# Performance work log

Hardware: AMD Instinct MI355X
Metric: run time of the kernel (lower is better)

Reference implementation:

```python
import jax, jax.numpy as jnp
import numpy as np

DIM = 1024; H = 16; KVH = 4; HD = 64          # head_dim = DIM // H
I = 2048                                       # intermediate_size = 2*DIM
N = 16                                         # ssm_state_size
DTR = 64                                       # dt_rank = DIM // 16
K = 4                                          # conv kernel
BASE = 10000.0
EPS = 1.1920929e-07                            # torch F.rms_norm default eps (fp32 finfo eps)

def rms_norm(x):
    return x * jax.lax.rsqrt(jnp.mean(x * x, axis=-1, keepdims=True) + EPS)

def rope_tables(S, dims):
    inv = 1.0 / BASE ** (jnp.arange(0, dims, 2, dtype=jnp.float32) / dims)
    f = jnp.outer(jnp.arange(S, dtype=jnp.float32), inv)   # [S, dims//2]
    return jnp.cos(f), jnp.sin(f)

def apply_rope(x, cos, sin):
    half = x.shape[-1] // 2
    x1, x2 = x[..., :half], x[..., half:]
    return jnp.concatenate([x1 * cos + x2 * sin, -x1 * sin + x2 * cos], axis=-1)

def setup_inputs() -> dict:
    key = jax.random.key(0)
    ks = jax.random.split(key, 12)
    B, S = 2, 2048
    def w(k, shape, s=0.02):
        return jax.random.normal(k, shape, jnp.float32) * s
    return {
        "x": jax.random.normal(ks[0], (B, S, DIM), jnp.float32),
        "W_mamba": w(ks[1], (2 * I, DIM)),
        "W_q": w(ks[2], (DIM, DIM)),
        "W_kv": w(ks[3], (2 * KVH * HD, DIM)),
        "q_gain": jnp.full((H,), 1.0, jnp.float32),
        "conv_w": w(ks[4], (I, K), 0.2),
        "conv_b": jnp.zeros((I,), jnp.float32),
        "W_xproj": w(ks[5], (DTR + 2 * N, I)),
        "W_dt": w(ks[6], (I, DTR)),
        "b_dt": w(ks[7], (I,), 0.5),
        "A_log": jnp.log(jnp.broadcast_to(jnp.arange(1, N + 1, dtype=jnp.float32), (I, N))),
        "D": jnp.ones((I,), jnp.float32),
        "W_mamba_out": w(ks[8], (DIM, I)),
        "W_proj": w(ks[9], (DIM, DIM)),
        "merge_alpha": jnp.zeros((1,), jnp.float32),
    }

def reference(x, W_mamba, W_q, W_kv, q_gain, conv_w, conv_b, W_xproj, W_dt, b_dt,
              A_log, D, W_mamba_out, W_proj, merge_alpha):
    B, S, _ = x.shape
    # --- parallel input projection for the mamba branch ---
    mp = x @ W_mamba.T                         # [B,S,2I]
    x_ssm, gate = mp[..., :I], mp[..., I:]
    # --- attention branch (GQA + full RoPE + per-head q gain) ---
    q = (x @ W_q.T).reshape(B, S, H, HD).transpose(0, 2, 1, 3)
    kv = x @ W_kv.T
    k = kv[..., :KVH * HD].reshape(B, S, KVH, HD).transpose(0, 2, 1, 3)
    v = kv[..., KVH * HD:].reshape(B, S, KVH, HD).transpose(0, 2, 1, 3)
    q = rms_norm(q); k = rms_norm(k)
    cos, sin = rope_tables(S, HD)
    q = apply_rope(q, cos, sin)
    k = apply_rope(k, cos, sin)
    q = q * q_gain[None, :, None, None]
    nrep = H // KVH
    k = jnp.repeat(k, nrep, axis=1)
    v = jnp.repeat(v, nrep, axis=1)
    scores = jnp.einsum('bhqd,bhkd->bhqk', q, k) / jnp.sqrt(jnp.float32(HD))
    mask = jnp.tril(jnp.ones((S, S), bool))
    scores = jnp.where(mask, scores, -jnp.inf)
    y = jnp.einsum('bhqk,bhkd->bhqd', jax.nn.softmax(scores, axis=-1), v)
    attn_out = y.transpose(0, 2, 1, 3).reshape(B, S, DIM)
    # --- mamba/SSM branch: causal depthwise conv1d + silu ---
    xc = x_ssm.transpose(0, 2, 1)              # [B,I,S]
    u = jax.lax.conv_general_dilated(xc, conv_w[:, None, :], (1,), [(K - 1, 0)],
                                     dimension_numbers=('NCH', 'OIH', 'NCH'),
                                     feature_group_count=I) + conv_b[None, :, None]
    u = u * jax.nn.sigmoid(u)                  # silu, [B,I,S]
    u_bsi = u.transpose(0, 2, 1)               # [B,S,I]
    params = u_bsi @ W_xproj.T                 # [B,S,DTR+2N]
    dt_low = params[..., :DTR]
    Bm = params[..., DTR:DTR + N]
    Cm = params[..., DTR + N:]
    delta = jax.nn.softplus(dt_low @ W_dt.T + b_dt)   # [B,S,I] (delta_bias + softplus)
    A = -jnp.exp(A_log)                        # [I,N]
    def step(state, inp):
        d_t, b_t, c_t, u_t = inp               # [B,I],[B,N],[B,N],[B,I]
        dA = jnp.exp(d_t[:, :, None] * A[None])
        state = state * dA + d_t[:, :, None] * b_t[:, None, :] * u_t[:, :, None]
        y_t = jnp.sum(state * c_t[:, None, :], axis=-1)
        return state, y_t
    xs = (delta.transpose(1, 0, 2), Bm.transpose(1, 0, 2),
          Cm.transpose(1, 0, 2), u_bsi.transpose(1, 0, 2))
    state0 = jnp.zeros((B, I, N), x.dtype)
    _, ys = jax.lax.scan(step, state0, xs)     # ys: [S,B,I]
    y_ssm = ys.transpose(1, 0, 2) + u_bsi * D  # + D skip
    y_ssm = y_ssm * (gate * jax.nn.sigmoid(gate))      # gated by silu(z)
    mamba_out = y_ssm @ W_mamba_out.T          # [B,S,DIM]
    # --- gated merge + output projection ---
    alpha = jax.nn.sigmoid(merge_alpha)
    merged = alpha * attn_out + (1.0 - alpha) * mamba_out
    return merged @ W_proj.T
```

## Files before the change

kernel.cpp:

```cpp
#include <hip/hip_runtime.h>
#include <hip/hip_bf16.h>

#define B_   2
#define S_   2048
#define T_   4096
#define DIM_ 1024
#define H_   16
#define KVH_ 4
#define HD_  64
#define I_   2048
#define N_   16
#define DTR_ 64
#define MB   ((size_t)1 << 20)

typedef __hip_bfloat16 bf16;
typedef __attribute__((ext_vector_type(8))) short short8;
typedef __attribute__((ext_vector_type(4))) short short4v;
typedef __attribute__((ext_vector_type(4))) float f32x4;

__device__ __forceinline__ float b2f(bf16 v){ return __bfloat162float(v); }
__device__ __forceinline__ bf16  f2b(float v){ return __float2bfloat16(v); }

__device__ __forceinline__ void async16(const void* g, void* l) {
  __builtin_amdgcn_global_load_lds((__attribute__((address_space(1))) void*)g,
                                   (__attribute__((address_space(3))) void*)l, 16, 0, 0);
}

__global__ __launch_bounds__(256)
void cast_f2b(const float* __restrict__ in, bf16* __restrict__ out, int n4)
{
  const int i = blockIdx.x * 256 + threadIdx.x;
  if (i >= n4) return;
  const float4 v = ((const float4*)in)[i];
  short4v o;
  o.x = (short)__builtin_bit_cast(unsigned short, f2b(v.x));
  o.y = (short)__builtin_bit_cast(unsigned short, f2b(v.y));
  o.z = (short)__builtin_bit_cast(unsigned short, f2b(v.z));
  o.w = (short)__builtin_bit_cast(unsigned short, f2b(v.w));
  *(short4v*)(out + (size_t)i * 4) = o;
}

template<int MODE>
__global__ __launch_bounds__(256)
void gemm_nt(const bf16* __restrict__ A, int lda,
             const bf16* __restrict__ W, int ldw,
             void* __restrict__ C, int ldc,
             const float* __restrict__ bias,
             int M, int N, int K)
{
  __shared__ __align__(16) bf16 As[128*32];
  __shared__ __align__(16) bf16 Bs[128*32];
  const int tid  = threadIdx.x;
  const int lane = tid & 63;
  const int wave = tid >> 6;
  const int l16  = lane & 15;
  const int quad = lane >> 4;
  const int wm   = (wave >> 1) << 6;
  const int wn   = (wave & 1) << 6;
  const int m0   = blockIdx.x << 7;
  const int n0   = blockIdx.y << 7;

  f32x4 acc[4][4];
  const f32x4 zero = {0.f, 0.f, 0.f, 0.f};
  #pragma unroll
  for (int i = 0; i < 4; i++)
    #pragma unroll
    for (int j = 0; j < 4; j++) acc[i][j] = zero;

  for (int k0 = 0; k0 < K; k0 += 32) {
    #pragma unroll
    for (int p = 0; p < 2; p++) {
      const int linear = ((p << 8) + tid) << 4;
      const int row    = linear >> 6;
      const int inrow  = linear & 63;
      async16(A + (size_t)(m0 + row) * lda + k0 + (inrow >> 1), (char*)As + linear);
      int wr = n0 + row; if (wr > N - 1) wr = N - 1;
      async16(W + (size_t)wr * ldw + k0 + (inrow >> 1), (char*)Bs + linear);
    }
    __syncthreads();
    short8 af[4], bfr[4];
    #pragma unroll
    for (int mt = 0; mt < 4; mt++)
      af[mt] = *(const short8*)((const char*)As + ((wm + (mt << 4) + l16) << 6) + (quad << 4));
    #pragma unroll
    for (int nt = 0; nt < 4; nt++)
      bfr[nt] = *(const short8*)((const char*)Bs + ((wn + (nt << 4) + l16) << 6) + (quad << 4));
    #pragma unroll
    for (int mt = 0; mt < 4; mt++)
      #pragma unroll
      for (int nt = 0; nt < 4; nt++)
        acc[mt][nt] = __builtin_amdgcn_mfma_f32_16x16x32_bf16(af[mt], bfr[nt], acc[mt][nt], 0, 0, 0);
    __syncthreads();
  }

  #pragma unroll
  for (int mt = 0; mt < 4; mt++) {
    #pragma unroll
    for (int nt = 0; nt < 4; nt++) {
      const int col = n0 + wn + (nt << 4) + l16;
      if (col >= N) continue;
      #pragma unroll
      for (int r = 0; r < 4; r++) {
        const int row = m0 + wm + (mt << 4) + (quad << 2) + r;
        float v = acc[mt][nt][r];
        if (MODE >= 2) {
          v += bias[col];
          v = (v > 20.f) ? v : log1pf(__expf(v));
        }
        if (MODE == 0 || MODE == 2) ((float*)C)[(size_t)row * ldc + col] = v;
        else                        ((bf16*)C)[(size_t)row * ldc + col] = f2b(v);
      }
    }
  }
}

__global__ __launch_bounds__(256)
void qkv_prep(const bf16* __restrict__ qraw, const bf16* __restrict__ kvraw,
              const float* __restrict__ q_gain,
              bf16* __restrict__ qn, bf16* __restrict__ kn, bf16* __restrict__ vt)
{
  const int wid  = blockIdx.x * 4 + (threadIdx.x >> 6);
  const int lane = threadIdx.x & 63;
  const int t    = wid / 24;
  const int slot = wid % 24;
  const int b = t >> 11, s = t & 2047;

  float val;
  if (slot < 16)       val = b2f(qraw [(size_t)t * 1024 + slot * 64 + lane]);
  else if (slot < 20)  val = b2f(kvraw[(size_t)t * 512  + (slot - 16) * 64 + lane]);
  else                 val = b2f(kvraw[(size_t)t * 512  + 256 + (slot - 20) * 64 + lane]);

  if (slot < 20) {
    float ss = val * val;
    #pragma unroll
    for (int off = 32; off; off >>= 1) ss += __shfl_xor(ss, off);
    val *= rsqrtf(ss * (1.0f / 64.0f) + 1.1920929e-07f);
    const int j = lane & 31;
    const float x1 = __shfl(val, j);
    const float x2 = __shfl(val, j + 32);
    const float inv = powf(10000.0f, -(float)j * (1.0f / 32.0f));
    const float ang = (float)s * inv;
    const float c = cosf(ang), sn = sinf(ang);
    val = (lane < 32) ? (x1 * c + x2 * sn) : (x2 * c - x1 * sn);
  }
  if (slot < 16) {
    val *= q_gain[slot];
    qn[((size_t)(b * 16 + slot) * 2048 + s) * 64 + lane] = f2b(val);
  } else if (slot < 20) {
    kn[((size_t)(b * 4 + (slot - 16)) * 2048 + s) * 64 + lane] = f2b(val);
  } else {
    vt[((size_t)(b * 4 + (slot - 20)) * 64 + lane) * 2048 + s] = f2b(val);
  }
}

__global__ __launch_bounds__(256)
void attn_fwd(const bf16* __restrict__ qn, const bf16* __restrict__ kn,
              const bf16* __restrict__ vt, bf16* __restrict__ attn)
{
  __shared__ __align__(16) bf16 Plds[4][16][32];
  const int b = blockIdx.z, h = blockIdx.y, q0 = blockIdx.x * 64;
  const int wave = threadIdx.x >> 6, lane = threadIdx.x & 63;
  const int l16 = lane & 15, quad = lane >> 4;
  const int kvh = h >> 2;
  const bf16* Q  = qn + (size_t)(b * 16 + h)   * 2048 * 64;
  const bf16* Kp = kn + (size_t)(b * 4 + kvh)  * 2048 * 64;
  const bf16* Vt = vt + (size_t)(b * 4 + kvh)  * 64 * 2048;

  const int qrow_l = q0 + wave * 16 + l16;
  const short8 qf0 = *(const short8*)(Q + (size_t)qrow_l * 64 + quad * 8);
  const short8 qf1 = *(const short8*)(Q + (size_t)qrow_l * 64 + 32 + quad * 8);

  f32x4 acc[4];
  const f32x4 zero = {0.f, 0.f, 0.f, 0.f};
  #pragma unroll
  for (int i = 0; i < 4; i++) acc[i] = zero;
  float m_r[4], l_r[4];
  #pragma unroll
  for (int r = 0; r < 4; r++) { m_r[r] = -1e30f; l_r[r] = 0.f; }

  const int nkt = (q0 + 64) >> 5;
  for (int kt = 0; kt < nkt; kt++) {
    const int kb = kt << 5;
    const short8 kfA0 = *(const short8*)(Kp + (size_t)(kb + l16) * 64 + quad * 8);
    const short8 kfA1 = *(const short8*)(Kp + (size_t)(kb + l16) * 64 + 32 + quad * 8);
    const short8 kfB0 = *(const short8*)(Kp + (size_t)(kb + 16 + l16) * 64 + quad * 8);
    const short8 kfB1 = *(const short8*)(Kp + (size_t)(kb + 16 + l16) * 64 + 32 + quad * 8);
    f32x4 sA = zero, sB = zero;
    sA = __builtin_amdgcn_mfma_f32_16x16x32_bf16(qf0, kfA0, sA, 0, 0, 0);
    sA = __builtin_amdgcn_mfma_f32_16x16x32_bf16(qf1, kfA1, sA, 0, 0, 0);
    sB = __builtin_amdgcn_mfma_f32_16x16x32_bf16(qf0, kfB0, sB, 0, 0, 0);
    sB = __builtin_amdgcn_mfma_f32_16x16x32_bf16(qf1, kfB1, sB, 0, 0, 0);

    const int colA = kb + l16, colB = kb + 16 + l16;
    float pA[4], pB[4], alpha[4];
    #pragma unroll
    for (int r = 0; r < 4; r++) {
      const int row = q0 + wave * 16 + quad * 4 + r;
      float a  = sA[r] * 0.125f;
      float bb = sB[r] * 0.125f;
      if (colA > row) a  = -1e30f;
      if (colB > row) bb = -1e30f;
      float tm = fmaxf(a, bb);
      #pragma unroll
      for (int off = 8; off; off >>= 1) tm = fmaxf(tm, __shfl_xor(tm, off));
      const float nm = fmaxf(m_r[r], tm);
      alpha[r] = __expf(m_r[r] - nm);
      m_r[r] = nm;
      const float pa = __expf(a - nm), pb = __expf(bb - nm);
      pA[r] = pa; pB[r] = pb;
      float ps = pa + pb;
      #pragma unroll
      for (int off = 8; off; off >>= 1) ps += __shfl_xor(ps, off);
      l_r[r] = l_r[r] * alpha[r] + ps;
    }
    #pragma unroll
    for (int nt = 0; nt < 4; nt++)
      #pragma unroll
      for (int r = 0; r < 4; r++) acc[nt][r] *= alpha[r];

    __syncthreads();
    #pragma unroll
    for (int r = 0; r < 4; r++) {
      Plds[wave][quad * 4 + r][l16]      = f2b(pA[r]);
      Plds[wave][quad * 4 + r][16 + l16] = f2b(pB[r]);
    }
    __syncthreads();
    const short8 pf = *(const short8*)(&Plds[wave][l16][quad * 8]);
    #pragma unroll
    for (int nt = 0; nt < 4; nt++) {
      const short8 vf = *(const short8*)(Vt + (size_t)(nt * 16 + l16) * 2048 + kb + quad * 8);
      acc[nt] = __builtin_amdgcn_mfma_f32_16x16x32_bf16(pf, vf, acc[nt], 0, 0, 0);
    }
  }

  #pragma unroll
  for (int nt = 0; nt < 4; nt++)
    #pragma unroll
    for (int r = 0; r < 4; r++) {
      const int row = q0 + wave * 16 + quad * 4 + r;
      attn[((size_t)b * 2048 + row) * 1024 + h * 64 + nt * 16 + l16] = f2b(acc[nt][r] / l_r[r]);
    }
}

__global__ __launch_bounds__(256)
void conv_silu(const bf16* __restrict__ xssm, const float* __restrict__ cw,
               const float* __restrict__ cb, bf16* __restrict__ u)
{
  const int i = blockIdx.x * 256 + threadIdx.x;
  const int t = blockIdx.y;
  const int s = t & 2047;
  float acc = cb[i];
  #pragma unroll
  for (int kk = 0; kk < 4; kk++) {
    const int sp = s - 3 + kk;
    if (sp >= 0) acc += b2f(xssm[(size_t)(t - 3 + kk) * 2048 + i]) * cw[i * 4 + kk];
  }
  const float sig = 1.f / (1.f + __expf(-acc));
  u[(size_t)t * 2048 + i] = f2b(acc * sig);
}

__global__ __launch_bounds__(256)
void ssm_scan(const bf16* __restrict__ delta, const bf16* __restrict__ u,
              const bf16* __restrict__ params, const float* __restrict__ A_log,
              const float* __restrict__ Dv, const bf16* __restrict__ gate,
              bf16* __restrict__ yout)
{
  __shared__ float Pl[16][17], Fl[16][17], Il[16][17];
  const int blk = blockIdx.x;
  const int b = blk >> 11, i = blk & 2047;
  const int n = threadIdx.x & 15, c = threadIdx.x >> 4;
  const float a  = -__expf(A_log[i * 16 + n]);
  const float Di = Dv[i];
  const size_t base = (size_t)b * 2048 + c * 128;

  float P = 1.f, F = 0.f;
  for (int j = 0; j < 128; j++) {
    const size_t rb = base + j;
    const float dt = b2f(delta[rb * 2048 + i]);
    const float ut = b2f(u[rb * 2048 + i]);
    const float Bn = b2f(params[rb * 96 + 64 + n]);
    const float dA = __expf(dt * a);
    P *= dA;
    F = F * dA + dt * ut * Bn;
  }
  Pl[n][c] = P; Fl[n][c] = F;
  __syncthreads();

  if (threadIdx.x < 16) {
    const int nn = threadIdx.x;
    float s = 0.f;
    #pragma unroll
    for (int cc = 0; cc < 16; cc++) {
      Il[nn][cc] = s;
      s = Fl[nn][cc] + Pl[nn][cc] * s;
    }
  }
  __syncthreads();

  float state = Il[n][c];
  for (int j = 0; j < 128; j++) {
    const size_t rb = base + j;
    const float dt = b2f(delta[rb * 2048 + i]);
    const float ut = b2f(u[rb * 2048 + i]);
    const float Bn = b2f(params[rb * 96 + 64 + n]);
    const float Cn = b2f(params[rb * 96 + 80 + n]);
    const float dA = __expf(dt * a);
    state = state * dA + dt * ut * Bn;
    float y = state * Cn;
    y += __shfl_xor(y, 1); y += __shfl_xor(y, 2);
    y += __shfl_xor(y, 4); y += __shfl_xor(y, 8);
    if (n == 0) {
      const float g  = b2f(gate[rb * 2048 + i]);
      const float gs = g / (1.f + __expf(-g));
      yout[rb * 2048 + i] = f2b((y + ut * Di) * gs);
    }
  }
}

__global__ __launch_bounds__(256)
void merge_k(const bf16* __restrict__ attn, const bf16* __restrict__ mamba,
             const float* __restrict__ malpha, bf16* __restrict__ merged)
{
  const size_t idx = (size_t)blockIdx.x * 256 + threadIdx.x;
  const float al = 1.f / (1.f + __expf(-malpha[0]));
  merged[idx] = f2b(al * b2f(attn[idx]) + (1.f - al) * b2f(mamba[idx]));
}

extern "C" void kernel_launch(void* const* d_in, const int* in_sizes, int n_in,
                              void* d_out, int out_size, void* d_ws, size_t ws_size,
                              hipStream_t stream)
{
  const float* x_f     = (const float*)d_in[0];
  const float* Wm_f    = (const float*)d_in[1];
  const float* Wq_f    = (const float*)d_in[2];
  const float* Wkv_f   = (const float*)d_in[3];
  const float* q_gain  = (const float*)d_in[4];
  const float* conv_w  = (const float*)d_in[5];
  const float* conv_b  = (const float*)d_in[6];
  const float* Wxp_f   = (const float*)d_in[7];
  const float* Wdt_f   = (const float*)d_in[8];
  const float* b_dt    = (const float*)d_in[9];
  const float* A_log   = (const float*)d_in[10];
  const float* Dv      = (const float*)d_in[11];
  const float* Wmo_f   = (const float*)d_in[12];
  const float* Wp_f    = (const float*)d_in[13];
  const float* malpha  = (const float*)d_in[14];

  char* wp = (char*)d_ws;
  bf16*  xb    = (bf16*)(wp + 0 * MB);
  bf16*  Wm_b  = (bf16*)(wp + 8 * MB);
  bf16*  Wq_b  = (bf16*)(wp + 16 * MB);
  bf16*  Wkv_b = (bf16*)(wp + 18 * MB);
  bf16*  xssm  = (bf16*)(wp + 19 * MB);
  bf16*  u     = (bf16*)(wp + 35 * MB);
  bf16*  gate  = (bf16*)(wp + 51 * MB);
  bf16*  qraw  = (bf16*)(wp + 67 * MB);
  bf16*  kvraw = (bf16*)(wp + 75 * MB);
  bf16*  dltb  = (bf16*)(wp + 79 * MB);
  bf16*  qn    = (bf16*)(wp + 0 * MB);
  bf16*  kn    = (bf16*)(wp + 8 * MB);
  bf16*  vtb   = (bf16*)(wp + 10 * MB);
  bf16*  Wxp_b = (bf16*)(wp + 12 * MB);
  bf16*  Wdt_b = (bf16*)(wp + 12 * MB + 512 * 1024);
  bf16*  prm   = (bf16*)(wp + 13 * MB);
  bf16*  Wp_b  = (bf16*)(wp + 14 * MB);
  bf16*  attnb = (bf16*)(wp + 67 * MB);
  bf16*  Wmo_b = (bf16*)(wp + 75 * MB);
  bf16*  ybuf  = (bf16*)(wp + 19 * MB);
  bf16*  mam   = (bf16*)(wp + 51 * MB);
  bf16*  mrg   = (bf16*)(wp + 59 * MB);
  (void)ws_size; (void)in_sizes; (void)n_in; (void)out_size;

  auto cast = [&](const float* src, bf16* dst, int n) {
    const int n4 = n >> 2;
    cast_f2b<<<dim3((n4 + 255) / 256), 256, 0, stream>>>(src, dst, n4);
  };
  cast(x_f,   xb,    T_ * 1024);
  cast(Wm_f,  Wm_b,  4096 * 1024);
  cast(Wq_f,  Wq_b,  1024 * 1024);
  cast(Wkv_f, Wkv_b, 512 * 1024);

  gemm_nt<1><<<dim3(32, 16), 256, 0, stream>>>(xb, 1024, Wm_b,               1024, xssm, 2048, nullptr, T_, 2048, 1024);
  gemm_nt<1><<<dim3(32, 16), 256, 0, stream>>>(xb, 1024, Wm_b + 2048 * 1024, 1024, gate, 2048, nullptr, T_, 2048, 1024);
  gemm_nt<1><<<dim3(32, 8),  256, 0, stream>>>(xb, 1024, Wq_b,  1024, qraw,  1024, nullptr, T_, 1024, 1024);
  gemm_nt<1><<<dim3(32, 4),  256, 0, stream>>>(xb, 1024, Wkv_b, 1024, kvraw,  512, nullptr, T_,  512, 1024);

  qkv_prep<<<dim3((T_ * 24) / 4), 256, 0, stream>>>(qraw, kvraw, q_gain, qn, kn, vtb);
  conv_silu<<<dim3(8, 4096), 256, 0, stream>>>(xssm, conv_w, conv_b, u);
  attn_fwd<<<dim3(32, 16, 2), 256, 0, stream>>>(qn, kn, vtb, attnb);

  cast(Wxp_f, Wxp_b, 96 * 2048);
  cast(Wdt_f, Wdt_b, 2048 * 64);
  cast(Wmo_f, Wmo_b, 1024 * 2048);
  cast(Wp_f,  Wp_b,  1024 * 1024);

  gemm_nt<1><<<dim3(32, 1),  256, 0, stream>>>(u, 2048, Wxp_b, 2048, prm, 96, nullptr, T_, 96, 2048);
  gemm_nt<3><<<dim3(32, 16), 256, 0, stream>>>(prm, 96, Wdt_b, 64, dltb, 2048, b_dt, T_, 2048, 64);
  ssm_scan<<<dim3(4096), 256, 0, stream>>>(dltb, u, prm, A_log, Dv, gate, ybuf);
  gemm_nt<1><<<dim3(32, 8),  256, 0, stream>>>(ybuf, 2048, Wmo_b, 2048, mam, 1024, nullptr, T_, 1024, 2048);

  merge_k<<<dim3(16384), 256, 0, stream>>>(attnb, mam, malpha, mrg);
  gemm_nt<0><<<dim3(32, 8),  256, 0, stream>>>(mrg, 1024, Wp_b, 1024, (float*)d_out, 1024, nullptr, T_, 1024, 1024);
}
```

Baseline: 1.046 ms.

## Store SSM scan inputs time-major and vectorize scan loads

```diff
diff --git a/kernel.cpp b/kernel.cpp
--- a/kernel.cpp
+++ b/kernel.cpp
@@ -20,6 +20,12 @@
 
 __device__ __forceinline__ float b2f(bf16 v){ return __bfloat162float(v); }
 __device__ __forceinline__ bf16  f2b(float v){ return __float2bfloat16(v); }
+__device__ __forceinline__ float s2f(short s){
+  return __builtin_bit_cast(float, ((unsigned int)(unsigned short)s) << 16);
+}
+__device__ __forceinline__ short f2s(float v){
+  return (short)__builtin_bit_cast(unsigned short, f2b(v));
+}
 
 __device__ __forceinline__ void async16(const void* g, void* l) {
   __builtin_amdgcn_global_load_lds((__attribute__((address_space(1))) void*)g,
@@ -33,18 +39,16 @@
   if (i >= n4) return;
   const float4 v = ((const float4*)in)[i];
   short4v o;
-  o.x = (short)__builtin_bit_cast(unsigned short, f2b(v.x));
-  o.y = (short)__builtin_bit_cast(unsigned short, f2b(v.y));
-  o.z = (short)__builtin_bit_cast(unsigned short, f2b(v.z));
-  o.w = (short)__builtin_bit_cast(unsigned short, f2b(v.w));
+  o.x = f2s(v.x); o.y = f2s(v.y); o.z = f2s(v.z); o.w = f2s(v.w);
   *(short4v*)(out + (size_t)i * 4) = o;
 }
 
-template<int MODE>
+template<int MODE, int TS>
 __global__ __launch_bounds__(256)
 void gemm_nt(const bf16* __restrict__ A, int lda,
              const bf16* __restrict__ W, int ldw,
              void* __restrict__ C, int ldc,
+             bf16* __restrict__ Ct, int ldt,
              const float* __restrict__ bias,
              int M, int N, int K)
 {
@@ -99,16 +103,29 @@
     for (int nt = 0; nt < 4; nt++) {
       const int col = n0 + wn + (nt << 4) + l16;
       if (col >= N) continue;
+      const int rowbase = m0 + wm + (mt << 4) + (quad << 2);
+      float v[4];
       #pragma unroll
       for (int r = 0; r < 4; r++) {
-        const int row = m0 + wm + (mt << 4) + (quad << 2) + r;
-        float v = acc[mt][nt][r];
-        if (MODE >= 2) {
-          v += bias[col];
-          v = (v > 20.f) ? v : log1pf(__expf(v));
+        float t = acc[mt][nt][r];
+        if (MODE == 2) {
+          t += bias[col];
+          t = (t > 20.f) ? t : log1pf(__expf(t));
         }
-        if (MODE == 0 || MODE == 2) ((float*)C)[(size_t)row * ldc + col] = v;
-        else                        ((bf16*)C)[(size_t)row * ldc + col] = f2b(v);
+        v[r] = t;
+      }
+      if (TS == 0 || TS == 2) {
+        #pragma unroll
+        for (int r = 0; r < 4; r++) {
+          if (MODE == 0) ((float*)C)[(size_t)(rowbase + r) * ldc + col] = v[r];
+          else           ((bf16*)C)[(size_t)(rowbase + r) * ldc + col] = f2b(v[r]);
+        }
+      }
+      if (TS >= 1) {
+        short4v p;
+        #pragma unroll
+        for (int r = 0; r < 4; r++) p[r] = f2s(v[r]);
+        *(short4v*)(Ct + (size_t)col * ldt + rowbase) = p;
       }
     }
   }
@@ -243,27 +260,58 @@
 }
 
 __global__ __launch_bounds__(256)
-void conv_silu(const bf16* __restrict__ xssm, const float* __restrict__ cw,
-               const float* __restrict__ cb, bf16* __restrict__ u)
-{
-  const int i = blockIdx.x * 256 + threadIdx.x;
-  const int t = blockIdx.y;
+void conv_silu_t(const bf16* __restrict__ xssmT, const float* __restrict__ cw,
+                 const float* __restrict__ cb,
+                 bf16* __restrict__ u, bf16* __restrict__ uT)
+{
+  const int i = blockIdx.x;
+  const int t = blockIdx.y * 256 + threadIdx.x;
   const int s = t & 2047;
   float acc = cb[i];
   #pragma unroll
   for (int kk = 0; kk < 4; kk++) {
-    const int sp = s - 3 + kk;
-    if (sp >= 0) acc += b2f(xssm[(size_t)(t - 3 + kk) * 2048 + i]) * cw[i * 4 + kk];
+    if (s - 3 + kk >= 0)
+      acc += s2f(__builtin_bit_cast(short, xssmT[(size_t)i * 4096 + t - 3 + kk])) * cw[i * 4 + kk];
   }
   const float sig = 1.f / (1.f + __expf(-acc));
-  u[(size_t)t * 2048 + i] = f2b(acc * sig);
-}
-
-__global__ __launch_bounds__(256)
-void ssm_scan(const bf16* __restrict__ delta, const bf16* __restrict__ u,
-              const bf16* __restrict__ params, const float* __restrict__ A_log,
-              const float* __restrict__ Dv, const bf16* __restrict__ gate,
-              bf16* __restrict__ yout)
+  const bf16 r = f2b(acc * sig);
+  u [(size_t)t * 2048 + i] = r;
+  uT[(size_t)i * 4096 + t] = r;
+}
+
+__global__ __launch_bounds__(256)
+void transpose_bf16(const bf16* __restrict__ in, bf16* __restrict__ out,
+                    int R, int C)
+{
+  __shared__ bf16 tile[64][65];
+  const int c0 = blockIdx.x * 64, r0 = blockIdx.y * 64;
+  #pragma unroll
+  for (int it = 0; it < 2; it++) {
+    const int linear = (it * 256 + threadIdx.x) * 8;
+    const int r = linear >> 6, cc = linear & 63;
+    const short8 v = *(const short8*)(in + (size_t)(r0 + r) * C + c0 + cc);
+    #pragma unroll
+    for (int k = 0; k < 8; k++)
+      tile[r][cc + k] = __builtin_bit_cast(bf16, (unsigned short)v[k]);
+  }
+  __syncthreads();
+  #pragma unroll
+  for (int it = 0; it < 2; it++) {
+    const int linear = (it * 256 + threadIdx.x) * 8;
+    const int oc = linear >> 6, k = linear & 63;
+    short8 v;
+    #pragma unroll
+    for (int kk = 0; kk < 8; kk++)
+      v[kk] = (short)__builtin_bit_cast(unsigned short, tile[k + kk][oc]);
+    *(short8*)(out + (size_t)(c0 + oc) * R + r0 + k) = v;
+  }
+}
+
+__global__ __launch_bounds__(256)
+void ssm_scan(const bf16* __restrict__ dltT, const bf16* __restrict__ uT,
+              const bf16* __restrict__ prmT, const float* __restrict__ A_log,
+              const float* __restrict__ Dv, const bf16* __restrict__ gateT,
+              bf16* __restrict__ youtT)
 {
   __shared__ float Pl[16][17], Fl[16][17], Il[16][17];
   const int blk = blockIdx.x;
@@ -271,17 +319,26 @@
   const int n = threadIdx.x & 15, c = threadIdx.x >> 4;
   const float a  = -__expf(A_log[i * 16 + n]);
   const float Di = Dv[i];
-  const size_t base = (size_t)b * 2048 + c * 128;
+  const size_t rowoff = (size_t)b * 2048 + c * 128;
+  const bf16* dp = dltT  + (size_t)i * 4096 + rowoff;
+  const bf16* up = uT    + (size_t)i * 4096 + rowoff;
+  const bf16* Bp = prmT  + (size_t)(64 + n) * 4096 + rowoff;
+  const bf16* Cp = prmT  + (size_t)(80 + n) * 4096 + rowoff;
+  const bf16* gp = gateT + (size_t)i * 4096 + rowoff;
+  bf16*       yp = youtT + (size_t)i * 4096 + rowoff;
 
   float P = 1.f, F = 0.f;
-  for (int j = 0; j < 128; j++) {
-    const size_t rb = base + j;
-    const float dt = b2f(delta[rb * 2048 + i]);
-    const float ut = b2f(u[rb * 2048 + i]);
-    const float Bn = b2f(params[rb * 96 + 64 + n]);
-    const float dA = __expf(dt * a);
-    P *= dA;
-    F = F * dA + dt * ut * Bn;
+  for (int j0 = 0; j0 < 128; j0 += 8) {
+    const short8 d8 = *(const short8*)(dp + j0);
+    const short8 u8 = *(const short8*)(up + j0);
+    const short8 B8 = *(const short8*)(Bp + j0);
+    #pragma unroll
+    for (int j = 0; j < 8; j++) {
+      const float dt = s2f(d8[j]);
+      const float dA = __expf(dt * a);
+      P *= dA;
+      F = F * dA + dt * s2f(u8[j]) * s2f(B8[j]);
+    }
   }
   Pl[n][c] = P; Fl[n][c] = F;
   __syncthreads();
@@ -298,22 +355,27 @@
   __syncthreads();
 
   float state = Il[n][c];
-  for (int j = 0; j < 128; j++) {
-    const size_t rb = base + j;
-    const float dt = b2f(delta[rb * 2048 + i]);
-    const float ut = b2f(u[rb * 2048 + i]);
-    const float Bn = b2f(params[rb * 96 + 64 + n]);
-    const float Cn = b2f(params[rb * 96 + 80 + n]);
-    const float dA = __expf(dt * a);
-    state = state * dA + dt * ut * Bn;
-    float y = state * Cn;
-    y += __shfl_xor(y, 1); y += __shfl_xor(y, 2);
-    y += __shfl_xor(y, 4); y += __shfl_xor(y, 8);
-    if (n == 0) {
-      const float g  = b2f(gate[rb * 2048 + i]);
+  for (int j0 = 0; j0 < 128; j0 += 8) {
+    const short8 d8 = *(const short8*)(dp + j0);
+    const short8 u8 = *(const short8*)(up + j0);
+    const short8 B8 = *(const short8*)(Bp + j0);
+    const short8 C8 = *(const short8*)(Cp + j0);
+    const short8 g8 = *(const short8*)(gp + j0);
+    short8 o8;
+    #pragma unroll
+    for (int j = 0; j < 8; j++) {
+      const float dt = s2f(d8[j]);
+      const float ut = s2f(u8[j]);
+      const float dA = __expf(dt * a);
+      state = state * dA + dt * ut * s2f(B8[j]);
+      float y = state * s2f(C8[j]);
+      y += __shfl_xor(y, 1); y += __shfl_xor(y, 2);
+      y += __shfl_xor(y, 4); y += __shfl_xor(y, 8);
+      const float g  = s2f(g8[j]);
       const float gs = g / (1.f + __expf(-g));
-      yout[rb * 2048 + i] = f2b((y + ut * Di) * gs);
-    }
+      o8[j] = f2s((y + ut * Di) * gs);
+    }
+    if (n == 0) *(short8*)(yp + j0) = o8;
   }
 }
 
@@ -351,24 +413,27 @@
   bf16*  Wm_b  = (bf16*)(wp + 8 * MB);
   bf16*  Wq_b  = (bf16*)(wp + 16 * MB);
   bf16*  Wkv_b = (bf16*)(wp + 18 * MB);
-  bf16*  xssm  = (bf16*)(wp + 19 * MB);
-  bf16*  u     = (bf16*)(wp + 35 * MB);
-  bf16*  gate  = (bf16*)(wp + 51 * MB);
-  bf16*  qraw  = (bf16*)(wp + 67 * MB);
-  bf16*  kvraw = (bf16*)(wp + 75 * MB);
-  bf16*  dltb  = (bf16*)(wp + 79 * MB);
+  bf16*  xssmT = (bf16*)(wp + 19 * MB);
+  bf16*  gateT = (bf16*)(wp + 35 * MB);
+  bf16*  u     = (bf16*)(wp + 51 * MB);
+  bf16*  uT    = (bf16*)(wp + 67 * MB);
+  bf16*  qraw  = (bf16*)(wp + 83 * MB);
+  bf16*  kvraw = (bf16*)(wp + 91 * MB);
+  bf16*  dltT  = (bf16*)(wp + 95 * MB);
   bf16*  qn    = (bf16*)(wp + 0 * MB);
   bf16*  kn    = (bf16*)(wp + 8 * MB);
   bf16*  vtb   = (bf16*)(wp + 10 * MB);
   bf16*  Wxp_b = (bf16*)(wp + 12 * MB);
   bf16*  Wdt_b = (bf16*)(wp + 12 * MB + 512 * 1024);
   bf16*  prm   = (bf16*)(wp + 13 * MB);
-  bf16*  Wp_b  = (bf16*)(wp + 14 * MB);
-  bf16*  attnb = (bf16*)(wp + 67 * MB);
-  bf16*  Wmo_b = (bf16*)(wp + 75 * MB);
+  bf16*  prmT  = (bf16*)(wp + 13 * MB + 768 * 1024);
+  bf16*  Wp_b  = (bf16*)(wp + 16 * MB);
+  bf16*  attnb = (bf16*)(wp + 83 * MB);
+  bf16*  Wmo_b = (bf16*)(wp + 91 * MB);
   bf16*  ybuf  = (bf16*)(wp + 19 * MB);
-  bf16*  mam   = (bf16*)(wp + 51 * MB);
-  bf16*  mrg   = (bf16*)(wp + 59 * MB);
+  bf16*  ybufT = (bf16*)(wp + 51 * MB);
+  bf16*  mam   = (bf16*)(wp + 35 * MB);
+  bf16*  mrg   = (bf16*)(wp + 43 * MB);
   (void)ws_size; (void)in_sizes; (void)n_in; (void)out_size;
 
   auto cast = [&](const float* src, bf16* dst, int n) {
@@ -380,13 +445,13 @@
   cast(Wq_f,  Wq_b,  1024 * 1024);
   cast(Wkv_f, Wkv_b, 512 * 1024);
 
-  gemm_nt<1><<<dim3(32, 16), 256, 0, stream>>>(xb, 1024, Wm_b,               1024, xssm, 2048, nullptr, T_, 2048, 1024);
-  gemm_nt<1><<<dim3(32, 16), 256, 0, stream>>>(xb, 1024, Wm_b + 2048 * 1024, 1024, gate, 2048, nullptr, T_, 2048, 1024);
-  gemm_nt<1><<<dim3(32, 8),  256, 0, stream>>>(xb, 1024, Wq_b,  1024, qraw,  1024, nullptr, T_, 1024, 1024);
-  gemm_nt<1><<<dim3(32, 4),  256, 0, stream>>>(xb, 1024, Wkv_b, 1024, kvraw,  512, nullptr, T_,  512, 1024);
+  gemm_nt<1,1><<<dim3(32, 16), 256, 0, stream>>>(xb, 1024, Wm_b,               1024, nullptr, 0, xssmT, 4096, nullptr, T_, 2048, 1024);
+  gemm_nt<1,1><<<dim3(32, 16), 256, 0, stream>>>(xb, 1024, Wm_b + 2048 * 1024, 1024, nullptr, 0, gateT, 4096, nullptr, T_, 2048, 1024);
+  gemm_nt<1,0><<<dim3(32, 8),  256, 0, stream>>>(xb, 1024, Wq_b,  1024, qraw,  1024, nullptr, 0, nullptr, T_, 1024, 1024);
+  gemm_nt<1,0><<<dim3(32, 4),  256, 0, stream>>>(xb, 1024, Wkv_b, 1024, kvraw,  512, nullptr, 0, nullptr, T_,  512, 1024);
 
   qkv_prep<<<dim3((T_ * 24) / 4), 256, 0, stream>>>(qraw, kvraw, q_gain, qn, kn, vtb);
-  conv_silu<<<dim3(8, 4096), 256, 0, stream>>>(xssm, conv_w, conv_b, u);
+  conv_silu_t<<<dim3(2048, 16), 256, 0, stream>>>(xssmT, conv_w, conv_b, u, uT);
   attn_fwd<<<dim3(32, 16, 2), 256, 0, stream>>>(qn, kn, vtb, attnb);
 
   cast(Wxp_f, Wxp_b, 96 * 2048);
@@ -394,11 +459,12 @@
   cast(Wmo_f, Wmo_b, 1024 * 2048);
   cast(Wp_f,  Wp_b,  1024 * 1024);
 
-  gemm_nt<1><<<dim3(32, 1),  256, 0, stream>>>(u, 2048, Wxp_b, 2048, prm, 96, nullptr, T_, 96, 2048);
-  gemm_nt<3><<<dim3(32, 16), 256, 0, stream>>>(prm, 96, Wdt_b, 64, dltb, 2048, b_dt, T_, 2048, 64);
-  ssm_scan<<<dim3(4096), 256, 0, stream>>>(dltb, u, prm, A_log, Dv, gate, ybuf);
-  gemm_nt<1><<<dim3(32, 8),  256, 0, stream>>>(ybuf, 2048, Wmo_b, 2048, mam, 1024, nullptr, T_, 1024, 2048);
+  gemm_nt<1,2><<<dim3(32, 1),  256, 0, stream>>>(u, 2048, Wxp_b, 2048, prm, 96, prmT, 4096, nullptr, T_, 96, 2048);
+  gemm_nt<2,1><<<dim3(32, 16), 256, 0, stream>>>(prm, 96, Wdt_b, 64, nullptr, 0, dltT, 4096, b_dt, T_, 2048, 64);
+  ssm_scan<<<dim3(4096), 256, 0, stream>>>(dltT, uT, prmT, A_log, Dv, gateT, ybufT);
+  transpose_bf16<<<dim3(64, 32), 256, 0, stream>>>(ybufT, ybuf, 2048, 4096);
+  gemm_nt<1,0><<<dim3(32, 8),  256, 0, stream>>>(ybuf, 2048, Wmo_b, 2048, mam, 1024, nullptr, 0, nullptr, T_, 1024, 2048);
 
   merge_k<<<dim3(16384), 256, 0, stream>>>(attnb, mam, malpha, mrg);
-  gemm_nt<0><<<dim3(32, 8),  256, 0, stream>>>(mrg, 1024, Wp_b, 1024, (float*)d_out, 1024, nullptr, T_, 1024, 1024);
-}
+  gemm_nt<0,0><<<dim3(32, 8),  256, 0, stream>>>(mrg, 1024, Wp_b, 1024, (float*)d_out, 1024, nullptr, 0, nullptr, T_, 1024, 1024);
+}
```

Measured after the change: 925.6 us. 11.5% less time.
